# Kernel optimization log

Hardware: AMD Instinct MI355X
Metric: run time of the kernel (lower is better)

The kernel has to match this reference:

```python
import jax, jax.numpy as jnp
import numpy as np

D_MODEL = 384; D_INNER = 768; D_STATE = 64; D_CONV = 4
HEADDIM = 48; NHEADS = 16; NLAYERS = 2
VOCAB = 4104  # 4098 (4096 6-mers + PAD/UNK) padded to multiple of 8
B, L = 32, 512
D_IN_PROJ = 2 * D_INNER + 2 * D_STATE + NHEADS  # 1664
CONV_DIM = D_INNER + 2 * D_STATE  # 896
N_ORDER, N_FAMILY, N_GENUS, N_SPECIES = 60, 427, 14216, 23964


def _layernorm(x, w, b, eps=1e-5):
    mu = jnp.mean(x, -1, keepdims=True)
    var = jnp.mean((x - mu) ** 2, -1, keepdims=True)
    return (x - mu) * jax.lax.rsqrt(var + eps) * w + b


def _mamba2(h, W_in, cw, cb, dtb, alog, d_skip, gw, W_out):
    b, l, _ = h.shape
    zxbcdt = h @ W_in                                  # (b,l,1664)
    z = zxbcdt[..., :D_INNER]
    xBC = zxbcdt[..., D_INNER:D_INNER + CONV_DIM]
    dt = zxbcdt[..., -NHEADS:]
    # causal depthwise conv1d (kernel D_CONV) + silu
    xp = jnp.pad(xBC, ((0, 0), (D_CONV - 1, 0), (0, 0)))
    conv = cb + sum(xp[:, k:k + l, :] * cw[:, k] for k in range(D_CONV))
    xBC = jax.nn.silu(conv)
    x = xBC[..., :D_INNER].reshape(b, l, NHEADS, HEADDIM)
    Bm = xBC[..., D_INNER:D_INNER + D_STATE]           # (b,l,n) ngroups=1
    Cm = xBC[..., D_INNER + D_STATE:]
    dt = jax.nn.softplus(dt + dtb)                     # (b,l,h)
    dA = jnp.exp(dt * (-jnp.exp(alog)))                # per-head scalar decay
    tm = lambda a: jnp.swapaxes(a, 0, 1)               # time-major for scan

    def step(state, inp):
        xt, dtt, dAt, Bt, Ct = inp                     # (b,h,p),(b,h),(b,h),(b,n),(b,n)
        state = state * dAt[:, :, None, None] + jnp.einsum('bhp,bn->bhpn', dtt[..., None] * xt, Bt)
        return state, jnp.einsum('bhpn,bn->bhp', state, Ct)

    state0 = jnp.zeros((b, NHEADS, HEADDIM, D_STATE), h.dtype)
    _, ys = jax.lax.scan(step, state0, (tm(x), tm(dt), tm(dA), tm(Bm), tm(Cm)))
    y = tm(ys) + d_skip[None, None, :, None] * x       # D skip per head
    y = y.reshape(b, l, D_INNER) * jax.nn.silu(z)      # gate
    y = y * jax.lax.rsqrt(jnp.mean(y * y, -1, keepdims=True) + 1e-5) * gw  # gated RMSNorm
    return y @ W_out


def setup_inputs():
    key = jax.random.key(0)
    ks = jax.random.split(key, 16)
    nrm = lambda k, s, sc=0.02: jax.random.normal(k, s, jnp.float32) * sc
    return {
        'tokens': jax.random.randint(ks[0], (B, L), 0, VOCAB),
        'emb': nrm(ks[1], (VOCAB, D_MODEL)),
        'ln_w': jnp.ones((NLAYERS, D_MODEL)), 'ln_b': jnp.zeros((NLAYERS, D_MODEL)),
        'in_proj_w': nrm(ks[2], (NLAYERS, D_MODEL, D_IN_PROJ)),
        'conv_w': nrm(ks[3], (NLAYERS, CONV_DIM, D_CONV), 0.1),
        'conv_b': jnp.zeros((NLAYERS, CONV_DIM)),
        'dt_bias': nrm(ks[4], (NLAYERS, NHEADS), 0.5),
        'A_log': jnp.log(jax.random.uniform(ks[5], (NLAYERS, NHEADS), minval=1.0, maxval=16.0)),
        'D': jnp.ones((NLAYERS, NHEADS)),
        'gnorm_w': jnp.ones((NLAYERS, D_INNER)),
        'out_proj_w': nrm(ks[6], (NLAYERS, D_INNER, D_MODEL)),
        'normf_w': jnp.ones((D_MODEL,)), 'normf_b': jnp.zeros((D_MODEL,)),
        'proj_ln_w': jnp.ones((D_MODEL,)), 'proj_ln_b': jnp.zeros((D_MODEL,)),
        'order_w': nrm(ks[7], (D_MODEL, N_ORDER)), 'order_b': jnp.zeros((N_ORDER,)),
        'family_w': nrm(ks[8], (D_MODEL, N_FAMILY)), 'family_b': jnp.zeros((N_FAMILY,)),
        'genus_w': nrm(ks[9], (D_MODEL, N_GENUS)), 'genus_b': jnp.zeros((N_GENUS,)),
        'species_w': nrm(ks[10], (D_MODEL, N_SPECIES)), 'species_b': jnp.zeros((N_SPECIES,)),
    }


def reference(tokens, emb, ln_w, ln_b, in_proj_w, conv_w, conv_b, dt_bias, A_log, D, gnorm_w, out_proj_w, normf_w, normf_b, proj_ln_w, proj_ln_b, order_w, order_b, family_w, family_b, genus_w, genus_b, species_w, species_b):
    resid = emb[tokens]                                # (B,L,d), embed dropout off (eval)
    for l in range(NLAYERS):                           # pre-norm residual blocks
        h = _layernorm(resid, ln_w[l], ln_b[l])
        resid = resid + _mamba2(h, in_proj_w[l], conv_w[l], conv_b[l], dt_bias[l], A_log[l], D[l], gnorm_w[l], out_proj_w[l])
    h = _layernorm(resid, normf_w, normf_b)            # norm_f -> hidden states
    feat = _layernorm(h.mean(axis=1), proj_ln_w, proj_ln_b)  # mean pool + shared LN (dropout eval)
    return jnp.concatenate([feat @ order_w + order_b,
                            feat @ family_w + family_b,
                            feat @ genus_w + genus_b,
                            feat @ species_w + species_b], axis=-1)
```

## Files before the change

kernel.cpp:

```cpp
#include <hip/hip_runtime.h>
#include <hip/hip_bf16.h>
#include <cmath>


#define B_SZ 32
#define L_SZ 512
#define DMODEL 384
#define DINNER 768
#define DSTATE 64
#define HEADDIM 48
#define NHEADS 16
#define DINPROJ 1680
#define CONVDIM 896
#define ROWS (B_SZ * L_SZ)
#define OUT_STRIDE 38667
#define NOUTPAD 38784
#define NCH 8
#define CHL (L_SZ / NCH)
#define N1PAD 1792

typedef __hip_bfloat16 bf16;
typedef unsigned short u16;
typedef __attribute__((ext_vector_type(8))) short bfrag;
typedef __attribute__((ext_vector_type(4))) float ffrag;

union BU { uint4 u; bfrag f; };

__device__ __forceinline__ float ldw(const void* p, size_t i, bool isb) {
    if (isb) return __bfloat162float(((const bf16*)p)[i]);
    else     return ((const float*)p)[i];
}

__device__ __forceinline__ short f2bs(float f) {
    unsigned u = __float_as_uint(f);
    u = u + 0x7FFFu + ((u >> 16) & 1u);
    return (short)(u >> 16);
}
__device__ __forceinline__ unsigned pk2(float a, float b) {
    return ((unsigned)(u16)f2bs(a)) | (((unsigned)(u16)f2bs(b)) << 16);
}
__device__ __forceinline__ float blo(unsigned u) { return __uint_as_float(u << 16); }
__device__ __forceinline__ float bhi(unsigned u) { return __uint_as_float(u & 0xFFFF0000u); }
__device__ __forceinline__ float bfv(u16 v) { return __uint_as_float(((unsigned)v) << 16); }

__device__ __forceinline__ void gl2lds16(const void* g, void* l) {
    __builtin_amdgcn_global_load_lds(
        (const __attribute__((address_space(1))) void*)g,
        (__attribute__((address_space(3))) void*)l, 16, 0, 0);
}

__global__ void detect_kernel(const void* __restrict__ ln_w, int* __restrict__ flag) {
    unsigned u = *(const unsigned*)ln_w;
    *flag = (u == 0x3F800000u) ? 0 : 1;
}

__global__ void embed_kernel(const int* __restrict__ tok,
                             const void* __restrict__ emb,
                             float* __restrict__ resid,
                             const int* __restrict__ dflag) {
    bool isb = (*dflag != 0);
    int r = blockIdx.x, d = threadIdx.x;
    resid[(size_t)r * DMODEL + d] = ldw(emb, (size_t)tok[r] * DMODEL + d, isb);
}

__global__ void layernorm_off(const float* __restrict__ x,
                              const void* __restrict__ w,
                              const void* __restrict__ b, long off,
                              void* __restrict__ out, int D, int obf,
                              const int* __restrict__ dflag) {
    bool isb = (*dflag != 0);
    int row = blockIdx.x, lane = threadIdx.x;
    const float* xr = x + (size_t)row * D;
    float s = 0.f, s2 = 0.f;
    for (int d = lane; d < D; d += 64) { float v = xr[d]; s += v; s2 += v * v; }
    #pragma unroll
    for (int o = 32; o; o >>= 1) { s += __shfl_xor(s, o); s2 += __shfl_xor(s2, o); }
    float mu = s / D;
    float var = s2 / D - mu * mu;
    float rinv = rsqrtf(var + 1e-5f);
    for (int d = lane; d < D; d += 64) {
        float v = (xr[d] - mu) * rinv * ldw(w, off + d, isb) + ldw(b, off + d, isb);
        if (obf) ((u16*)out)[(size_t)row * D + d] = (u16)f2bs(v);
        else     ((float*)out)[(size_t)row * D + d] = v;
    }
}

__global__ void transpose_w(const void* __restrict__ W, long woff,
                            int K, int N, u16* __restrict__ WT, int NT,
                            const int* __restrict__ dflag) {
    bool isb = (*dflag != 0);
    __shared__ float t[64][65];
    int n0 = blockIdx.x * 64, k0 = blockIdx.y * 64;
    for (int i = threadIdx.x; i < 4096; i += 256) {
        int kk = i >> 6, nn = i & 63;
        int gk = k0 + kk, gn = n0 + nn;
        float v = (gn < N && gk < K) ? ldw(W, woff + (size_t)gk * N + gn, isb) : 0.f;
        t[nn][kk] = v;
    }
    __syncthreads();
    for (int i = threadIdx.x; i < 4096; i += 256) {
        int nn = i >> 6, kk = i & 63;
        int gn = n0 + nn, gk = k0 + kk;
        if (gn < NT && gk < K)
            WT[(size_t)gn * K + gk] = (u16)f2bs(t[nn][kk]);
    }
}

__global__ __launch_bounds__(256)
void gemm128(const u16* __restrict__ A, int lda,
             const u16* __restrict__ BT, int ldb,
             float* __restrict__ C, int ldc,
             const float* __restrict__ Cadd,
             int M, int N, int K,
             const float* __restrict__ bias, int obf) {
    __shared__ u16 As[128 * 64];
    __shared__ u16 Bs[128 * 64];
    const int tid = threadIdx.x, lane = tid & 63, w = tid >> 6;
    const int bm = blockIdx.y * 128, bn = blockIdx.x * 128;
    const int wr = w >> 1, wc = w & 1;
    ffrag acc[4][4];
    #pragma unroll
    for (int i = 0; i < 4; ++i)
        #pragma unroll
        for (int j = 0; j < 4; ++j) acc[i][j] = 0.f;

    const int sr = lane >> 3;
    const int swz = (((lane & 7) ^ sr) << 4) >> 1;
    const u16* Asrc = A + (size_t)bm * lda + swz;
    const u16* Bsrc = BT + (size_t)bn * ldb + swz;

    for (int k0 = 0; k0 < K; k0 += 64) {
        #pragma unroll
        for (int i = 0; i < 4; ++i) {
            int r = w * 32 + i * 8 + sr;
            gl2lds16(Asrc + (size_t)r * lda + k0, &As[(w * 32 + i * 8) * 64]);
            gl2lds16(Bsrc + (size_t)r * ldb + k0, &Bs[(w * 32 + i * 8) * 64]);
        }
        __syncthreads();
        #pragma unroll
        for (int ks = 0; ks < 2; ++ks) {
            bfrag af[4], bf[4];
            #pragma unroll
            for (int mi = 0; mi < 4; ++mi) {
                int rr = wr * 64 + mi * 16 + (lane & 15);
                int byte = (rr * 128 + ks * 64 + (lane >> 4) * 16) ^ ((rr & 7) << 4);
                af[mi] = *(const bfrag*)&As[byte >> 1];
            }
            #pragma unroll
            for (int ni = 0; ni < 4; ++ni) {
                int rr = wc * 64 + ni * 16 + (lane & 15);
                int byte = (rr * 128 + ks * 64 + (lane >> 4) * 16) ^ ((rr & 7) << 4);
                bf[ni] = *(const bfrag*)&Bs[byte >> 1];
            }
            #pragma unroll
            for (int mi = 0; mi < 4; ++mi)
                #pragma unroll
                for (int ni = 0; ni < 4; ++ni)
                    acc[mi][ni] = __builtin_amdgcn_mfma_f32_16x16x32_bf16(
                        af[mi], bf[ni], acc[mi][ni], 0, 0, 0);
        }
        __syncthreads();
    }
    int col = lane & 15, r0 = (lane >> 4) * 4;
    #pragma unroll
    for (int mi = 0; mi < 4; ++mi)
        #pragma unroll
        for (int ni = 0; ni < 4; ++ni) {
            int gn = bn + wc * 64 + ni * 16 + col;
            if (gn < N) {
                float bv = bias ? bias[gn] : 0.f;
                #pragma unroll
                for (int r = 0; r < 4; ++r) {
                    int gm = bm + wr * 64 + mi * 16 + r0 + r;
                    if (gm < M) {
                        size_t idx = (size_t)gm * ldc + gn;
                        float v = acc[mi][ni][r] + bv;
                        if (obf) {
                            ((u16*)C)[idx] = (u16)f2bs(v);
                        } else {
                            if (Cadd) v += Cadd[idx];
                            C[idx] = v;
                        }
                    }
                }
            }
        }
}

__global__ __launch_bounds__(256)
void conv_fuse(const u16* __restrict__ zxb,
               const void* __restrict__ cw, const void* __restrict__ cb,
               long cwoff, long cboff,
               float* __restrict__ convb,
               u16* __restrict__ xT,
               const int* __restrict__ dflag) {
    bool isb = (*dflag != 0);
    int tid = threadIdx.x;
    if (tid >= 224) return;
    int bk = blockIdx.x;
    int b = bk >> 6;
    int l0 = (bk & 63) * 8;
    int c0 = tid * 4;
    const u16* zbase = zxb + (size_t)b * L_SZ * DINPROJ + DINNER;
    float cwv[4][4], cbv[4];
    #pragma unroll
    for (int j = 0; j < 4; ++j) {
        cbv[j] = ldw(cb, cboff + c0 + j, isb);
        #pragma unroll
        for (int k = 0; k < 4; ++k)
            cwv[j][k] = ldw(cw, cwoff + (size_t)(c0 + j) * 4 + k, isb);
    }
    uint2 rw[11];
    #pragma unroll
    for (int i = 0; i < 11; ++i) {
        int lsrc = l0 - 3 + i;
        rw[i] = (lsrc >= 0) ? *(const uint2*)&zbase[(size_t)lsrc * DINPROJ + c0]
                            : make_uint2(0u, 0u);
    }
    float out[8][4];
    #pragma unroll
    for (int t = 0; t < 8; ++t) {
        float i0[4] = {blo(rw[t].x),     bhi(rw[t].x),     blo(rw[t].y),     bhi(rw[t].y)};
        float i1[4] = {blo(rw[t+1].x),   bhi(rw[t+1].x),   blo(rw[t+1].y),   bhi(rw[t+1].y)};
        float i2[4] = {blo(rw[t+2].x),   bhi(rw[t+2].x),   blo(rw[t+2].y),   bhi(rw[t+2].y)};
        float i3[4] = {blo(rw[t+3].x),   bhi(rw[t+3].x),   blo(rw[t+3].y),   bhi(rw[t+3].y)};
        #pragma unroll
        for (int j = 0; j < 4; ++j) {
            float acc = cbv[j] + i0[j] * cwv[j][0] + i1[j] * cwv[j][1]
                               + i2[j] * cwv[j][2] + i3[j] * cwv[j][3];
            out[t][j] = acc / (1.f + expf(-acc));
        }
    }
    size_t rowbase = (size_t)b * L_SZ + l0;
    if (c0 < DINNER) {
        #pragma unroll
        for (int t = 0; t < 8; ++t)
            *(float4*)&convb[(rowbase + t) * CONVDIM + c0] =
                make_float4(out[t][0], out[t][1], out[t][2], out[t][3]);
        int cch = l0 >> 6, tg = (l0 >> 3) & 7;
        u16* xdst = xT + (size_t)(b * NCH + cch) * 49152 + tg * 6144;
        #pragma unroll
        for (int j = 0; j < 4; ++j) {
            uint4 pk;
            pk.x = pk2(out[0][j], out[1][j]);
            pk.y = pk2(out[2][j], out[3][j]);
            pk.z = pk2(out[4][j], out[5][j]);
            pk.w = pk2(out[6][j], out[7][j]);
            *(uint4*)(xdst + (size_t)(c0 + j) * 8) = pk;
        }
    } else {
        #pragma unroll
        for (int t = 0; t < 8; ++t) {
            uint2 pk;
            pk.x = pk2(out[t][0], out[t][1]);
            pk.y = pk2(out[t][2], out[t][3]);
            *(uint2*)((u16*)(convb + (rowbase + t) * CONVDIM + DINNER) + (c0 - DINNER)) = pk;
        }
    }
}

__global__ void dt_off(const u16* __restrict__ zxb,
                       const void* __restrict__ dtb,
                       long hoff,
                       float* __restrict__ dtout,
                       const int* __restrict__ dflag) {
    bool isb = (*dflag != 0);
    int idx = blockIdx.x * 256 + threadIdx.x;
    int r = idx >> 4, h = idx & 15;
    float x = bfv(zxb[(size_t)r * DINPROJ + (DINPROJ - NHEADS) + h]) + ldw(dtb, hoff + h, isb);
    float sp = (x > 20.f) ? x : log1pf(expf(x));
    dtout[idx] = sp;
}


__global__ __launch_bounds__(512)
void scan_p1(const float* __restrict__ convbc,
             const float* __restrict__ dtg,
             const void* __restrict__ alog, long hoff,
             const u16* __restrict__ xT,
             float* __restrict__ sendb, float* __restrict__ Pbuf,
             const int* __restrict__ dflag) {
    bool isb = (*dflag != 0);
    int c = blockIdx.x & (NCH - 1);
    int hg = (blockIdx.x >> 3) & 1;
    int b = blockIdx.x >> 4;
    int lane = threadIdx.x & 63;
    int wv = threadIdx.x >> 6;
    int h = hg * 8 + wv;
    int slotC = b * NCH + c;
    int slotS = (b << 7) | (h << 3) | c;
    __shared__ __align__(16) u16 BT[64][72];
    __shared__ __align__(16) float La[8][64];
    __shared__ __align__(16) float Dt[8][64];
    #pragma unroll
    for (int it = 0; it < 8; ++it) {
        int idx = it * 512 + threadIdx.x;
        int t = idx >> 6, n = idx & 63;
        BT[n][t] = *((const u16*)(convbc + (size_t)(slotC * 64 + t) * CONVDIM + DINNER) + n);
    }
    float dtv = dtg[((size_t)slotC * 64 + lane) * NHEADS + h];
    float A = expf(ldw(alog, hoff + h, isb));
    float cs = dtv;
    #pragma unroll
    for (int o = 1; o < 64; o <<= 1) { float v = __shfl_up(cs, o); if (lane >= o) cs += v; }
    La[wv][lane] = -A * cs;
    Dt[wv][lane] = dtv;
    __syncthreads();
    float la63 = La[wv][63];
    ffrag acc[3][4];
    #pragma unroll
    for (int i = 0; i < 3; ++i)
        #pragma unroll
        for (int j = 0; j < 4; ++j) acc[i][j] = 0.f;
    #pragma unroll
    for (int ks = 0; ks < 2; ++ks) {
        int t0 = ks * 32 + (lane >> 4) * 8;
        float4 lA = *(const float4*)&La[wv][t0];
        float4 lB = *(const float4*)&La[wv][t0 + 4];
        float4 dA4 = *(const float4*)&Dt[wv][t0];
        float4 dB4 = *(const float4*)&Dt[wv][t0 + 4];
        float v0 = expf(la63 - lA.x) * dA4.x;
        float v1 = expf(la63 - lA.y) * dA4.y;
        float v2 = expf(la63 - lA.z) * dA4.z;
        float v3 = expf(la63 - lA.w) * dA4.w;
        float v4 = expf(la63 - lB.x) * dB4.x;
        float v5 = expf(la63 - lB.y) * dB4.y;
        float v6 = expf(la63 - lB.z) * dB4.z;
        float v7 = expf(la63 - lB.w) * dB4.w;
        BU xv[3];
        #pragma unroll
        for (int ni = 0; ni < 3; ++ni) {
            int p = h * 48 + (lane & 15) + 16 * ni;
            uint4 raw = *(const uint4*)(xT + (size_t)slotC * 49152 + (t0 >> 3) * 6144 + p * 8);
            xv[ni].u.x = pk2(blo(raw.x) * v0, bhi(raw.x) * v1);
            xv[ni].u.y = pk2(blo(raw.y) * v2, bhi(raw.y) * v3);
            xv[ni].u.z = pk2(blo(raw.z) * v4, bhi(raw.z) * v5);
            xv[ni].u.w = pk2(blo(raw.w) * v6, bhi(raw.w) * v7);
        }
        #pragma unroll
        for (int nj = 0; nj < 4; ++nj) {
            bfrag bt = *(const bfrag*)&BT[(lane & 15) + 16 * nj][t0];
            #pragma unroll
            for (int mi = 0; mi < 3; ++mi)
                acc[mi][nj] = __builtin_amdgcn_mfma_f32_16x16x32_bf16(
                    xv[mi].f, bt, acc[mi][nj], 0, 0, 0);
        }
    }
    float* sb = sendb + (size_t)slotS * 3072;
    #pragma unroll
    for (int mi = 0; mi < 3; ++mi)
        #pragma unroll
        for (int nj = 0; nj < 4; ++nj)
            #pragma unroll
            for (int r = 0; r < 4; ++r) {
                int p = 16 * mi + (lane >> 4) * 4 + r;
                int n = 16 * nj + (lane & 15);
                sb[p * 64 + n] = acc[mi][nj][r];
            }
    if (lane == 0) Pbuf[slotS] = expf(la63);
}

__global__ void scan_p2(float* __restrict__ sendb, const float* __restrict__ Pbuf) {
    int bh = blockIdx.x;
    int lane = threadIdx.x;
    float4 S[12];
    #pragma unroll
    for (int q = 0; q < 12; ++q) S[q] = make_float4(0.f, 0.f, 0.f, 0.f);
    for (int c = 0; c < NCH - 1; ++c) {
        int s = bh * NCH + c;
        float P = Pbuf[s];
        #pragma unroll
        for (int q = 0; q < 12; ++q) {
            float4* p = (float4*)&sendb[(size_t)s * 3072 + 4 * lane + 256 * q];
            float4 L = *p;
            S[q].x = S[q].x * P + L.x;
            S[q].y = S[q].y * P + L.y;
            S[q].z = S[q].z * P + L.z;
            S[q].w = S[q].w * P + L.w;
            *p = S[q];
        }
    }
}

__global__ __launch_bounds__(512)
void scan_p3(float* __restrict__ convb,
             const float* __restrict__ dtg,
             const void* __restrict__ alog,
             const void* __restrict__ Dsk, long hoff,
             const u16* __restrict__ xT,
             const float* __restrict__ sendb,
             const int* __restrict__ dflag) {
    bool isb = (*dflag != 0);
    int c = blockIdx.x & (NCH - 1);
    int hg = (blockIdx.x >> 3) & 1;
    int b = blockIdx.x >> 4;
    int lane = threadIdx.x & 63;
    int wv = threadIdx.x >> 6;
    int h = hg * 8 + wv;
    int slotC = b * NCH + c;
    int slotS = (b << 7) | (h << 3) | c;
    __shared__ __align__(16) u16 Bl[64][72];
    __shared__ __align__(16) u16 Cl[64][72];
    __shared__ __align__(16) float Gl[64][68];
    __shared__ __align__(16) float La[8][64];
    __shared__ __align__(16) float Dt[8][64];
    #pragma unroll
    for (int it = 0; it < 2; ++it) {
        int idx = it * 512 + threadIdx.x;
        int r = idx >> 4, c8 = (idx & 15) * 8;
        uint4 v = *(const uint4*)((const u16*)(convb + (size_t)(slotC * 64 + r) * CONVDIM + DINNER) + c8);
        if (c8 < 64) *(uint4*)&Bl[r][c8] = v;
        else         *(uint4*)&Cl[r][c8 - 64] = v;
    }
    float dtv = dtg[((size_t)slotC * 64 + lane) * NHEADS + h];
    float A = expf(ldw(alog, hoff + h, isb));
    float cs = dtv;
    #pragma unroll
    for (int o = 1; o < 64; o <<= 1) { float v = __shfl_up(cs, o); if (lane >= o) cs += v; }
    La[wv][lane] = -A * cs;
    Dt[wv][lane] = dtv;
    __syncthreads();
    if (wv < 4) {
        ffrag g[4];
        #pragma unroll
        for (int j = 0; j < 4; ++j) g[j] = 0.f;
        #pragma unroll
        for (int ks = 0; ks < 2; ++ks) {
            int k0 = ks * 32 + (lane >> 4) * 8;
            bfrag af = *(const bfrag*)&Cl[wv * 16 + (lane & 15)][k0];
            #pragma unroll
            for (int nj = 0; nj < 4; ++nj) {
                bfrag bf = *(const bfrag*)&Bl[(lane & 15) + 16 * nj][k0];
                g[nj] = __builtin_amdgcn_mfma_f32_16x16x32_bf16(af, bf, g[nj], 0, 0, 0);
            }
        }
        #pragma unroll
        for (int nj = 0; nj < 4; ++nj)
            #pragma unroll
            for (int r = 0; r < 4; ++r)
                Gl[wv * 16 + (lane >> 4) * 4 + r][16 * nj + (lane & 15)] = g[nj][r];
    }
    __syncthreads();
    float dskip = ldw(Dsk, hoff + h, isb);
    BU xf[3][2];
    #pragma unroll
    for (int ks = 0; ks < 2; ++ks) {
        int tg = ks * 4 + (lane >> 4);
        #pragma unroll
        for (int ni = 0; ni < 3; ++ni) {
            int p = h * 48 + (lane & 15) + 16 * ni;
            xf[ni][ks].u = *(const uint4*)(xT + (size_t)slotC * 49152 + tg * 6144 + p * 8);
        }
    }
    ffrag aY[4][3];
    #pragma unroll
    for (int i = 0; i < 4; ++i)
        #pragma unroll
        for (int j = 0; j < 3; ++j) aY[i][j] = 0.f;
    #pragma unroll
    for (int ks = 0; ks < 2; ++ks) {
        int t0 = ks * 32 + (lane >> 4) * 8;
        float4 lA = *(const float4*)&La[wv][t0];
        float4 lB = *(const float4*)&La[wv][t0 + 4];
        float4 dA4 = *(const float4*)&Dt[wv][t0];
        float4 dB4 = *(const float4*)&Dt[wv][t0 + 4];
        #pragma unroll
        for (int mi = 0; mi < 4; ++mi) {
            int tloc = (lane & 15) + 16 * mi;
            float lat = La[wv][tloc];
            float4 g0 = *(const float4*)&Gl[tloc][t0];
            float4 g1 = *(const float4*)&Gl[tloc][t0 + 4];
            float m0 = (t0 + 0 <= tloc) ? expf(lat - lA.x) * dA4.x * g0.x : 0.f;
            float m1 = (t0 + 1 <= tloc) ? expf(lat - lA.y) * dA4.y * g0.y : 0.f;
            float m2 = (t0 + 2 <= tloc) ? expf(lat - lA.z) * dA4.z * g0.z : 0.f;
            float m3 = (t0 + 3 <= tloc) ? expf(lat - lA.w) * dA4.w * g0.w : 0.f;
            float m4 = (t0 + 4 <= tloc) ? expf(lat - lB.x) * dB4.x * g1.x : 0.f;
            float m5 = (t0 + 5 <= tloc) ? expf(lat - lB.y) * dB4.y * g1.y : 0.f;
            float m6 = (t0 + 6 <= tloc) ? expf(lat - lB.z) * dB4.z * g1.z : 0.f;
            float m7 = (t0 + 7 <= tloc) ? expf(lat - lB.w) * dB4.w * g1.w : 0.f;
            BU mf;
            mf.u.x = pk2(m0, m1); mf.u.y = pk2(m2, m3);
            mf.u.z = pk2(m4, m5); mf.u.w = pk2(m6, m7);
            #pragma unroll
            for (int ni = 0; ni < 3; ++ni)
                aY[mi][ni] = __builtin_amdgcn_mfma_f32_16x16x32_bf16(
                    mf.f, xf[ni][ks].f, aY[mi][ni], 0, 0, 0);
        }
    }
    if (c > 0) {
        const float* sb = sendb + (size_t)(slotS - 1) * 3072;
        #pragma unroll
        for (int ks = 0; ks < 2; ++ks) {
            int n0 = ks * 32 + (lane >> 4) * 8;
            BU s0[3];
            #pragma unroll
            for (int ni = 0; ni < 3; ++ni) {
                int p = (lane & 15) + 16 * ni;
                const float* sp = sb + p * 64 + n0;
                float4 sa = *(const float4*)sp;
                float4 sbv = *(const float4*)(sp + 4);
                s0[ni].u.x = pk2(sa.x, sa.y); s0[ni].u.y = pk2(sa.z, sa.w);
                s0[ni].u.z = pk2(sbv.x, sbv.y); s0[ni].u.w = pk2(sbv.z, sbv.w);
            }
            #pragma unroll
            for (int mi = 0; mi < 4; ++mi) {
                int tloc = (lane & 15) + 16 * mi;
                float u = expf(La[wv][tloc]);
                BU crU; crU.f = *(const bfrag*)&Cl[tloc][n0];
                BU csc;
                csc.u.x = pk2(blo(crU.u.x) * u, bhi(crU.u.x) * u);
                csc.u.y = pk2(blo(crU.u.y) * u, bhi(crU.u.y) * u);
                csc.u.z = pk2(blo(crU.u.z) * u, bhi(crU.u.z) * u);
                csc.u.w = pk2(blo(crU.u.w) * u, bhi(crU.u.w) * u);
                #pragma unroll
                for (int ni = 0; ni < 3; ++ni)
                    aY[mi][ni] = __builtin_amdgcn_mfma_f32_16x16x32_bf16(
                        csc.f, s0[ni].f, aY[mi][ni], 0, 0, 0);
            }
        }
    }
    #pragma unroll
    for (int mi = 0; mi < 4; ++mi)
        #pragma unroll
        for (int ni = 0; ni < 3; ++ni)
            #pragma unroll
            for (int r = 0; r < 4; ++r) {
                int t = 16 * mi + (lane >> 4) * 4 + r;
                size_t idx = (size_t)(slotC * 64 + t) * CONVDIM + h * 48 + 16 * ni + (lane & 15);
                float x = convb[idx];
                convb[idx] = aY[mi][ni][r] + dskip * x;
            }
}

__global__ void gated_off(float* __restrict__ y,
                          const u16* __restrict__ zxb,
                          const void* __restrict__ gw, long goff,
                          const int* __restrict__ dflag) {
    bool isb = (*dflag != 0);
    int row = blockIdx.x, tid = threadIdx.x;
    float* yr = y + (size_t)row * CONVDIM;
    const u16* zr = zxb + (size_t)row * DINPROJ;
    float g[3], s2 = 0.f;
    #pragma unroll
    for (int i = 0; i < 3; ++i) {
        int d = tid + 256 * i;
        float z = bfv(zr[d]);
        float sz = z / (1.f + expf(-z));
        float v = yr[d] * sz;
        g[i] = v; s2 += v * v;
    }
    #pragma unroll
    for (int o = 32; o; o >>= 1) s2 += __shfl_xor(s2, o);
    __shared__ float red[4];
    if ((tid & 63) == 0) red[tid >> 6] = s2;
    __syncthreads();
    s2 = red[0] + red[1] + red[2] + red[3];
    float rinv = rsqrtf(s2 / (float)DINNER + 1e-5f);
    u16* yb = (u16*)yr;
    #pragma unroll
    for (int i = 0; i < 3; ++i) {
        int d = tid + 256 * i;
        yb[d] = (u16)f2bs(g[i] * rinv * ldw(gw, goff + d, isb));
    }
}

__global__ void pool_part(const float* __restrict__ h, float* __restrict__ part) {
    int b = blockIdx.x, g = blockIdx.y, d = threadIdx.x;
    const float* hp = h + ((size_t)b * L_SZ + g * 64) * DMODEL + d;
    float s = 0.f;
    #pragma unroll 8
    for (int l = 0; l < 64; ++l) s += hp[(size_t)l * DMODEL];
    part[((size_t)b * 8 + g) * DMODEL + d] = s;
}
__global__ void pool_final(const float* __restrict__ part, float* __restrict__ feat0) {
    int b = blockIdx.x, d = threadIdx.x;
    float s = 0.f;
    #pragma unroll
    for (int g = 0; g < 8; ++g) s += part[((size_t)b * 8 + g) * DMODEL + d];
    feat0[b * DMODEL + d] = s * (1.f / L_SZ);
}

__global__ void biascat(const void* __restrict__ bo, const void* __restrict__ bf_,
                        const void* __restrict__ bg, const void* __restrict__ bs,
                        float* __restrict__ biasAll, const int* __restrict__ dflag) {
    bool isb = (*dflag != 0);
    int j = blockIdx.x * 256 + threadIdx.x;
    if (j >= OUT_STRIDE) return;
    float v;
    if (j < 60)        v = ldw(bo, j, isb);
    else if (j < 487)  v = ldw(bf_, j - 60, isb);
    else if (j < 14703) v = ldw(bg, j - 487, isb);
    else               v = ldw(bs, j - 14703, isb);
    biasAll[j] = v;
}
__global__ void pad_feat(const float* __restrict__ feat, u16* __restrict__ featp) {
    int r = blockIdx.x, d = threadIdx.x;
    featp[r * DMODEL + d] = (r < B_SZ) ? (u16)f2bs(feat[r * DMODEL + d]) : (u16)0;
}
__global__ void zero_wpad(u16* __restrict__ WhT) {
    int r = blockIdx.x, d = threadIdx.x;
    WhT[(size_t)(OUT_STRIDE + r) * DMODEL + d] = 0;
}

extern "C" void kernel_launch(void* const* d_in, const int* in_sizes, int n_in,
                              void* d_out, int out_size, void* d_ws, size_t ws_size,
                              hipStream_t stream) {
    const int*  tokens   = (const int*)d_in[0];
    const void* emb      = d_in[1];
    const void* ln_w     = d_in[2];
    const void* ln_b     = d_in[3];
    const void* in_proj  = d_in[4];
    const void* conv_w   = d_in[5];
    const void* conv_b   = d_in[6];
    const void* dt_bias  = d_in[7];
    const void* A_log    = d_in[8];
    const void* Dp       = d_in[9];
    const void* gnorm_w  = d_in[10];
    const void* out_proj = d_in[11];
    const void* normf_w  = d_in[12];
    const void* normf_b  = d_in[13];
    const void* pln_w    = d_in[14];
    const void* pln_b    = d_in[15];
    const void* order_w  = d_in[16];
    const void* order_b  = d_in[17];
    const void* family_w = d_in[18];
    const void* family_b = d_in[19];
    const void* genus_w  = d_in[20];
    const void* genus_b  = d_in[21];
    const void* species_w= d_in[22];
    const void* species_b= d_in[23];
    float* out = (float*)d_out;

    float* ws    = (float*)d_ws;
    float* resid = ws;
    float* hbuf  = resid + (size_t)ROWS * DMODEL;
    u16*   zxb   = (u16*)(hbuf + (size_t)ROWS * DMODEL);
    float* sendb = (float*)(zxb + (size_t)ROWS * DINPROJ);
    float* convb = sendb + (size_t)4096 * 3072;
    float* dtb_  = convb + (size_t)ROWS * CONVDIM;
    float* dAb   = dtb_  + (size_t)ROWS * NHEADS;
    float* feat0 = dAb   + (size_t)ROWS * NHEADS;
    float* feat  = feat0 + (size_t)B_SZ * DMODEL;
    float* Pbuf  = feat  + (size_t)B_SZ * DMODEL;
    int*   dflag = (int*)(Pbuf + 4096);
    u16*   W1T   = (u16*)(Pbuf + 4096 + 16);
    u16*   W2T   = W1T + (size_t)2 * N1PAD * DMODEL;
    float* ppart = sendb;
    u16*   xT    = (u16*)hbuf;
    u16*   WhT   = zxb;
    u16*   featp = (u16*)dAb;
    float* biasAll = (float*)(featp + 128 * DMODEL);

    detect_kernel<<<1, 1, 0, stream>>>(ln_w, dflag);
    embed_kernel<<<ROWS, DMODEL, 0, stream>>>(tokens, emb, resid, dflag);
    biascat<<<(OUT_STRIDE + 255) / 256, 256, 0, stream>>>(
        order_b, family_b, genus_b, species_b, biasAll, dflag);

    for (int l = 0; l < 2; ++l) {
        transpose_w<<<dim3(N1PAD / 64, DMODEL / 64), 256, 0, stream>>>(
            in_proj, (long)l * DMODEL * DINPROJ, DMODEL, DINPROJ,
            W1T + (size_t)l * N1PAD * DMODEL, N1PAD, dflag);
        transpose_w<<<dim3(DMODEL / 64, DINNER / 64), 256, 0, stream>>>(
            out_proj, (long)l * DINNER * DMODEL, DINNER, DMODEL,
            W2T + (size_t)l * DMODEL * DINNER, DMODEL, dflag);
    }

    for (int l = 0; l < 2; ++l) {
        layernorm_off<<<ROWS, 64, 0, stream>>>(resid, ln_w, ln_b,
            (long)l * DMODEL, hbuf, DMODEL, 1, dflag);
        gemm128<<<dim3(N1PAD / 128, ROWS / 128), 256, 0, stream>>>(
            (const u16*)hbuf, DMODEL,
            W1T + (size_t)l * N1PAD * DMODEL, DMODEL,
            (float*)zxb, DINPROJ, nullptr, ROWS, DINPROJ, DMODEL, nullptr, 1);
        conv_fuse<<<B_SZ * 64, 256, 0, stream>>>(
            zxb, conv_w, conv_b, (long)l * CONVDIM * 4, (long)l * CONVDIM,
            convb, xT, dflag);
        dt_off<<<(ROWS * NHEADS) / 256, 256, 0, stream>>>(
            zxb, dt_bias, (long)l * NHEADS, dtb_, dflag);
        scan_p1<<<B_SZ * 2 * NCH, 512, 0, stream>>>(convb, dtb_, A_log,
            (long)l * NHEADS, xT, sendb, Pbuf, dflag);
        scan_p2<<<B_SZ * NHEADS, 64, 0, stream>>>(sendb, Pbuf);
        scan_p3<<<B_SZ * 2 * NCH, 512, 0, stream>>>(convb, dtb_, A_log, Dp,
            (long)l * NHEADS, xT, sendb, dflag);
        gated_off<<<ROWS, 256, 0, stream>>>(convb, zxb, gnorm_w,
            (long)l * DINNER, dflag);
        gemm128<<<dim3(DMODEL / 128, ROWS / 128), 256, 0, stream>>>(
            (const u16*)convb, CONVDIM * 2,
            W2T + (size_t)l * DMODEL * DINNER, DINNER,
            resid, DMODEL, resid, ROWS, DMODEL, DINNER, nullptr, 0);
    }

    transpose_w<<<dim3(1, 6), 256, 0, stream>>>(
        order_w, 0L, DMODEL, 60, WhT, 60, dflag);
    transpose_w<<<dim3(7, 6), 256, 0, stream>>>(
        family_w, 0L, DMODEL, 427, WhT + (size_t)60 * DMODEL, 427, dflag);
    transpose_w<<<dim3(223, 6), 256, 0, stream>>>(
        genus_w, 0L, DMODEL, 14216, WhT + (size_t)487 * DMODEL, 14216, dflag);
    transpose_w<<<dim3(375, 6), 256, 0, stream>>>(
        species_w, 0L, DMODEL, 23964, WhT + (size_t)14703 * DMODEL, 23964, dflag);
    zero_wpad<<<NOUTPAD - OUT_STRIDE, DMODEL, 0, stream>>>(WhT);

    layernorm_off<<<ROWS, 64, 0, stream>>>(resid, normf_w, normf_b, 0L,
                                           hbuf, DMODEL, 0, dflag);
    pool_part<<<dim3(B_SZ, 8), DMODEL, 0, stream>>>(hbuf, ppart);
    pool_final<<<B_SZ, DMODEL, 0, stream>>>(ppart, feat0);
    layernorm_off<<<B_SZ, 64, 0, stream>>>(feat0, pln_w, pln_b, 0L,
                                           feat, DMODEL, 0, dflag);
    pad_feat<<<128, DMODEL, 0, stream>>>(feat, featp);

    gemm128<<<dim3(NOUTPAD / 128, 1), 256, 0, stream>>>(
        featp, DMODEL, WhT, DMODEL,
        out, OUT_STRIDE, nullptr, B_SZ, OUT_STRIDE, DMODEL, biasAll, 0);
}
```

Before: 762.0 us.

## Fuse dt softplus into conv kernel, remap GEMM blocks per XCD, pack bf16 stores

The separate dt_off kernel is removed. Its softplus work now runs in the 32 previously idle threads of each conv_fuse block, which saves one launch and one pass over zxb per layer. The GEMM remaps block indices so that contiguous row tiles land on the same XCD, aiming at better L2 reuse of the B operand. Its bf16 epilogue also pairs adjacent columns via a lane shuffle into 32-bit stores. The risk is that the extra shuffle and the remapping add overhead if the L2 locality does not improve.

```diff
diff --git a/kernel.cpp b/kernel.cpp
--- a/kernel.cpp
+++ b/kernel.cpp
@@ -116,7 +116,14 @@
     __shared__ u16 As[128 * 64];
     __shared__ u16 Bs[128 * 64];
     const int tid = threadIdx.x, lane = tid & 63, w = tid >> 6;
-    const int bm = blockIdx.y * 128, bn = blockIdx.x * 128;
+    int bxl = blockIdx.x, byl = blockIdx.y;
+    if ((gridDim.y & 7) == 0) {
+        int L = byl * gridDim.x + bxl;
+        int xcd = L & 7, idx = L >> 3;
+        byl = xcd * (gridDim.y >> 3) + idx / gridDim.x;
+        bxl = idx % gridDim.x;
+    }
+    const int bm = byl * 128, bn = bxl * 128;
     const int wr = w >> 1, wc = w & 1;
     ffrag acc[4][4];
     #pragma unroll
@@ -167,21 +174,19 @@
         #pragma unroll
         for (int ni = 0; ni < 4; ++ni) {
             int gn = bn + wc * 64 + ni * 16 + col;
-            if (gn < N) {
-                float bv = bias ? bias[gn] : 0.f;
-                #pragma unroll
-                for (int r = 0; r < 4; ++r) {
-                    int gm = bm + wr * 64 + mi * 16 + r0 + r;
-                    if (gm < M) {
-                        size_t idx = (size_t)gm * ldc + gn;
-                        float v = acc[mi][ni][r] + bv;
-                        if (obf) {
-                            ((u16*)C)[idx] = (u16)f2bs(v);
-                        } else {
-                            if (Cadd) v += Cadd[idx];
-                            C[idx] = v;
-                        }
-                    }
+            float bv = (bias && gn < N) ? bias[gn] : 0.f;
+            #pragma unroll
+            for (int r = 0; r < 4; ++r) {
+                int gm = bm + wr * 64 + mi * 16 + r0 + r;
+                float v = acc[mi][ni][r] + bv;
+                if (obf) {
+                    float vn = __shfl_xor(v, 1);
+                    if (!(lane & 1) && gn < N && gm < M)
+                        *(unsigned*)&((u16*)C)[(size_t)gm * ldc + gn] = pk2(v, vn);
+                } else if (gn < N && gm < M) {
+                    size_t idx = (size_t)gm * ldc + gn;
+                    if (Cadd) v += Cadd[idx];
+                    C[idx] = v;
                 }
             }
         }
@@ -191,15 +196,32 @@
 void conv_fuse(const u16* __restrict__ zxb,
                const void* __restrict__ cw, const void* __restrict__ cb,
                long cwoff, long cboff,
+               const void* __restrict__ dtb, long hoff,
                float* __restrict__ convb,
                u16* __restrict__ xT,
+               float* __restrict__ dtout,
                const int* __restrict__ dflag) {
     bool isb = (*dflag != 0);
     int tid = threadIdx.x;
-    if (tid >= 224) return;
     int bk = blockIdx.x;
     int b = bk >> 6;
     int l0 = (bk & 63) * 8;
+    size_t rowbase = (size_t)b * L_SZ + l0;
+    if (tid >= 224) {
+        int i = tid - 224;
+        int rr = i >> 2, hq = (i & 3) * 4;
+        size_t row = rowbase + rr;
+        float4 sp;
+        float* spp = (float*)&sp;
+        #pragma unroll
+        for (int j = 0; j < 4; ++j) {
+            float x = bfv(zxb[row * DINPROJ + (DINPROJ - NHEADS) + hq + j]) +
+                      ldw(dtb, hoff + hq + j, isb);
+            spp[j] = (x > 20.f) ? x : log1pf(expf(x));
+        }
+        *(float4*)&dtout[row * NHEADS + hq] = sp;
+        return;
+    }
     int c0 = tid * 4;
     const u16* zbase = zxb + (size_t)b * L_SZ * DINPROJ + DINNER;
     float cwv[4][4], cbv[4];
@@ -231,7 +253,6 @@
             out[t][j] = acc / (1.f + expf(-acc));
         }
     }
-    size_t rowbase = (size_t)b * L_SZ + l0;
     if (c0 < DINNER) {
         #pragma unroll
         for (int t = 0; t < 8; ++t)
@@ -257,19 +278,6 @@
             *(uint2*)((u16*)(convb + (rowbase + t) * CONVDIM + DINNER) + (c0 - DINNER)) = pk;
         }
     }
-}
-
-__global__ void dt_off(const u16* __restrict__ zxb,
-                       const void* __restrict__ dtb,
-                       long hoff,
-                       float* __restrict__ dtout,
-                       const int* __restrict__ dflag) {
-    bool isb = (*dflag != 0);
-    int idx = blockIdx.x * 256 + threadIdx.x;
-    int r = idx >> 4, h = idx & 15;
-    float x = bfv(zxb[(size_t)r * DINPROJ + (DINPROJ - NHEADS) + h]) + ldw(dtb, hoff + h, isb);
-    float sp = (x > 20.f) ? x : log1pf(expf(x));
-    dtout[idx] = sp;
 }
 
 
@@ -674,9 +682,7 @@
             (float*)zxb, DINPROJ, nullptr, ROWS, DINPROJ, DMODEL, nullptr, 1);
         conv_fuse<<<B_SZ * 64, 256, 0, stream>>>(
             zxb, conv_w, conv_b, (long)l * CONVDIM * 4, (long)l * CONVDIM,
-            convb, xT, dflag);
-        dt_off<<<(ROWS * NHEADS) / 256, 256, 0, stream>>>(
-            zxb, dt_bias, (long)l * NHEADS, dtb_, dflag);
+            dt_bias, (long)l * NHEADS, convb, xT, dtb_, dflag);
         scan_p1<<<B_SZ * 2 * NCH, 512, 0, stream>>>(convb, dtb_, A_log,
             (long)l * NHEADS, xT, sendb, Pbuf, dflag);
         scan_p2<<<B_SZ * NHEADS, 64, 0, stream>>>(sendb, Pbuf);
```

Result: no change. 756.0 us (-0.8%).
